# Optimization experiments

Hardware: AMD Instinct MI355X
Metric: run time of the kernel (lower is better)

Reference implementation:

```python
import jax, jax.numpy as jnp
import numpy as np

N_NODES = 50000
N_EDGES = 800000
N_GRAPHS = 128
HEADS = 4
NEG_SLOPE = 0.2


def gat_layer(x, src, dst, W, a_src, a_dst, b, n_nodes):
    # x: [N, Fin]; W: [Fin, H*Fout]; a_src/a_dst: [H, Fout]; b: [H*Fout]
    H, Fo = a_src.shape
    h = (x @ W).reshape(n_nodes, H, Fo)                      # [N, H, Fo]
    s_src = jnp.einsum('nhf,hf->nh', h, a_src)               # [N, H]
    s_dst = jnp.einsum('nhf,hf->nh', h, a_dst)               # [N, H]
    e = jax.nn.leaky_relu(s_src[src] + s_dst[dst], NEG_SLOPE)  # [E, H]
    # segment softmax over destination nodes
    emax = jax.ops.segment_max(e, dst, num_segments=n_nodes)
    ex = jnp.exp(e - emax[dst])
    denom = jax.ops.segment_sum(ex, dst, num_segments=n_nodes)
    alpha = ex / (denom[dst] + 1e-16)                        # [E, H]
    msg = h[src] * alpha[:, :, None]                         # [E, H, Fo]
    out = jax.ops.segment_sum(msg, dst, num_segments=n_nodes)
    return out.reshape(n_nodes, H * Fo) + b


def setup_inputs() -> dict:
    key = jax.random.key(0)
    ks = jax.random.split(key, 16)
    x = jax.random.normal(ks[0], (N_NODES, 128), dtype=jnp.float32)
    edge_index = jax.random.randint(ks[1], (2, N_EDGES), 0, N_NODES, dtype=jnp.int64 if jax.config.jax_enable_x64 else jnp.int32)
    batch_index = jnp.sort(jax.random.randint(ks[2], (N_NODES,), 0, N_GRAPHS))
    s = 0.1
    # layer 0: in=128 -> H=4, Fo=32  => hidden 128
    W0 = jax.random.normal(ks[3], (128, HEADS * 32), jnp.float32) * s
    a_src0 = jax.random.normal(ks[4], (HEADS, 32), jnp.float32) * s
    a_dst0 = jax.random.normal(ks[5], (HEADS, 32), jnp.float32) * s
    b0 = jnp.zeros((HEADS * 32,), jnp.float32)
    # layer 1: in=128 -> H=4, Fo=64 => hidden 256
    W1 = jax.random.normal(ks[6], (128, HEADS * 64), jnp.float32) * s
    a_src1 = jax.random.normal(ks[7], (HEADS, 64), jnp.float32) * s
    a_dst1 = jax.random.normal(ks[8], (HEADS, 64), jnp.float32) * s
    b1 = jnp.zeros((HEADS * 64,), jnp.float32)
    # layer 2: in=256 -> H=4, Fo=64 => hidden 256
    W2 = jax.random.normal(ks[9], (256, HEADS * 64), jnp.float32) * s
    a_src2 = jax.random.normal(ks[10], (HEADS, 64), jnp.float32) * s
    a_dst2 = jax.random.normal(ks[11], (HEADS, 64), jnp.float32) * s
    b2 = jnp.zeros((HEADS * 64,), jnp.float32)
    # readout linear: 512 -> 10
    Wout = jax.random.normal(ks[12], (512, 10), jnp.float32) * s
    bout = jnp.zeros((10,), jnp.float32)
    return dict(x=x, edge_index=edge_index, batch_index=batch_index,
                W0=W0, a_src0=a_src0, a_dst0=a_dst0, b0=b0,
                W1=W1, a_src1=a_src1, a_dst1=a_dst1, b1=b1,
                W2=W2, a_src2=a_src2, a_dst2=a_dst2, b2=b2,
                Wout=Wout, bout=bout)


def reference(x, edge_index, batch_index,
              W0, a_src0, a_dst0, b0,
              W1, a_src1, a_dst1, b1,
              W2, a_src2, a_dst2, b2,
              Wout, bout):
    n = x.shape[0]
    loops = jnp.arange(n, dtype=edge_index.dtype)
    src = jnp.concatenate([edge_index[0], loops])  # PyG add_self_loops
    dst = jnp.concatenate([edge_index[1], loops])
    h = jax.nn.relu(gat_layer(x, src, dst, W0, a_src0, a_dst0, b0, n))
    h = jax.nn.relu(gat_layer(h, src, dst, W1, a_src1, a_dst1, b1, n))
    h = jax.nn.relu(gat_layer(h, src, dst, W2, a_src2, a_dst2, b2, n))
    # global mean / max pool per graph
    ssum = jax.ops.segment_sum(h, batch_index, num_segments=N_GRAPHS)
    cnt = jax.ops.segment_sum(jnp.ones((n, 1), h.dtype), batch_index, num_segments=N_GRAPHS)
    gmean = ssum / jnp.maximum(cnt, 1.0)
    gmax = jax.ops.segment_max(h, batch_index, num_segments=N_GRAPHS)
    pooled = jnp.concatenate([gmean, gmax], axis=1)  # [G, 512]
    return pooled @ Wout + bout
```

## Files before the change

kernel.cpp:

```cpp
#include <hip/hip_runtime.h>
#include <cfloat>

#define N_NODES 50000
#define N_EDGES 800000
#define E_TOT   850000
#define NG      128
#define NH      4
#define CHUNK   782

typedef float f4 __attribute__((ext_vector_type(4)));
typedef float v4f __attribute__((ext_vector_type(4)));
typedef _Float16 h8v __attribute__((ext_vector_type(8)));

__global__ void count_dst_k(const int* __restrict__ ei, int* __restrict__ cnt) {
    int e = blockIdx.x * blockDim.x + threadIdx.x;
    if (e >= E_TOT) return;
    int d = (e < N_EDGES) ? ei[N_EDGES + e] : (e - N_EDGES);
    atomicAdd(&cnt[d], 1);
}

__global__ void scan_sums_k(const int* __restrict__ cnt, int* __restrict__ bsum) {
    int b = blockIdx.x;
    int start = b * CHUNK, end2 = min(start + CHUNK, N_NODES);
    int lane = threadIdx.x & 63, wv = threadIdx.x >> 6;
    int s = 0;
    for (int i = start + threadIdx.x; i < end2; i += 256) s += cnt[i];
    #pragma unroll
    for (int off = 32; off; off >>= 1) s += __shfl_xor(s, off);
    __shared__ int ws[4];
    if (lane == 0) ws[wv] = s;
    __syncthreads();
    if (threadIdx.x == 0) bsum[b] = ws[0] + ws[1] + ws[2] + ws[3];
}

__global__ void scan_off_k(int* __restrict__ bsum, int* __restrict__ row_ptr) {
    int lane = threadIdx.x;
    int v = bsum[lane];
    int s = v;
    #pragma unroll
    for (int off = 1; off < 64; off <<= 1) {
        int t = __shfl_up(s, off);
        if (lane >= off) s += t;
    }
    bsum[lane] = s - v;
    if (lane == 63) row_ptr[N_NODES] = s;
}

__global__ void scan_write_k(const int* __restrict__ cnt, const int* __restrict__ bsum,
                             int* __restrict__ row_ptr, int* __restrict__ cursor) {
    int b = blockIdx.x;
    int start = b * CHUNK, end2 = min(start + CHUNK, N_NODES);
    __shared__ int wsum[4];
    __shared__ int carry_sh;
    int lane = threadIdx.x & 63, wv = threadIdx.x >> 6;
    if (threadIdx.x == 0) carry_sh = bsum[b];
    __syncthreads();
    for (int base = start; base < end2; base += 256) {
        int i = base + threadIdx.x;
        int v = (i < end2) ? cnt[i] : 0;
        int s = v;
        #pragma unroll
        for (int off = 1; off < 64; off <<= 1) {
            int t = __shfl_up(s, off);
            if (lane >= off) s += t;
        }
        if (lane == 63) wsum[wv] = s;
        __syncthreads();
        int woff = 0;
        #pragma unroll
        for (int k = 0; k < 4; ++k) if (k < wv) woff += wsum[k];
        int carry = carry_sh;
        if (i < end2) { int rp = carry + woff + s - v; row_ptr[i] = rp; cursor[i] = rp; }
        __syncthreads();
        if (threadIdx.x == 0) carry_sh = carry + wsum[0] + wsum[1] + wsum[2] + wsum[3];
        __syncthreads();
    }
}

__global__ void fill_k(const int* __restrict__ ei, int* __restrict__ cursor,
                       int* __restrict__ col) {
    int e = blockIdx.x * blockDim.x + threadIdx.x;
    if (e >= E_TOT) return;
    int s, d;
    if (e < N_EDGES) { s = ei[e]; d = ei[N_EDGES + e]; }
    else { s = e - N_EDGES; d = s; }
    int slot = atomicAdd(&cursor[d], 1);
    col[slot] = s;
}

template<int K, int NOUT>
__global__ void pack_w_k(const float* __restrict__ W, _Float16* __restrict__ Wp) {
    constexpr int total = (NOUT / 16) * (K / 32) * 64;
    int t = blockIdx.x * blockDim.x + threadIdx.x;
    if (t >= total) return;
    int lane = t & 63;
    int rest = t >> 6;
    int ks = rest % (K / 32);
    int n  = rest / (K / 32);
    int colW = n * 16 + (lane & 15);
    int krow = ks * 32 + (lane >> 4) * 8;
    h8v v;
    #pragma unroll
    for (int j = 0; j < 8; ++j) v[j] = (_Float16)W[(size_t)(krow + j) * NOUT + colW];
    *(h8v*)(Wp + (size_t)t * 8) = v;
}

template<int K, int NOUT>
__global__ void pack_a_k(const float* __restrict__ W, const float* __restrict__ asrc,
                         const float* __restrict__ adst, _Float16* __restrict__ Wp) {
    constexpr int KS = K / 32;
    constexpr int NT = NOUT / 16;
    constexpr int Fo = NOUT / NH;
    int t = blockIdx.x * blockDim.x + threadIdx.x;
    if (t >= KS * 64) return;
    int ks = t >> 6, lane = t & 63;
    int colL = lane & 15;
    int krow = ks * 32 + ((lane >> 4) & 3) * 8;
    h8v v = {};
    if (colL < 8) {
        int hd = colL & 3;
        const float* av = (colL < 4) ? asrc : adst;
        #pragma unroll
        for (int j = 0; j < 8; ++j) {
            float s = 0.f;
            const float* wr = W + (size_t)(krow + j) * NOUT + hd * Fo;
            for (int f = 0; f < Fo; ++f) s += wr[f] * av[hd * Fo + f];
            v[j] = (_Float16)s;
        }
    }
    *(h8v*)(Wp + (size_t)((NT * KS + ks) * 64 + lane) * 8) = v;
}

template<int K, int NOUT, typename XT>
__global__ __launch_bounds__(256) void gemm_k(const XT* __restrict__ x,
                                              const _Float16* __restrict__ Wp,
                                              _Float16* __restrict__ outh,
                                              float* __restrict__ ssrc,
                                              float* __restrict__ sdst) {
    constexpr int SLICE = NOUT / 8;
    constexpr int KS  = K / 32;
    constexpr int NT  = NOUT / 16;
    constexpr int LK  = K + 8;
    __shared__ __align__(16) _Float16 xs[64 * LK];
    int row0 = blockIdx.x * 64;
    for (int seg = threadIdx.x; seg < 64 * K / 8; seg += 256) {
        int r = seg / (K / 8);
        int c = (seg % (K / 8)) * 8;
        h8v v = {};
        if (row0 + r < N_NODES) {
            if constexpr (sizeof(XT) == 2) {
                v = *(const h8v*)((const _Float16*)x + (size_t)(row0 + r) * K + c);
            } else {
                const float* xp = (const float*)x + (size_t)(row0 + r) * K + c;
                float4 a = *(const float4*)xp;
                float4 b = *(const float4*)(xp + 4);
                v[0] = (_Float16)a.x; v[1] = (_Float16)a.y;
                v[2] = (_Float16)a.z; v[3] = (_Float16)a.w;
                v[4] = (_Float16)b.x; v[5] = (_Float16)b.y;
                v[6] = (_Float16)b.z; v[7] = (_Float16)b.w;
            }
        }
        *(h8v*)(xs + r * LK + c) = v;
    }
    __syncthreads();
    int wv = threadIdx.x >> 6, lane = threadIdx.x & 63;
    int quad = lane >> 4, colL = lane & 15;
    int r0 = row0 + wv * 16;
    h8v afr[KS];
    #pragma unroll
    for (int ks = 0; ks < KS; ++ks)
        afr[ks] = *(const h8v*)(xs + (wv * 16 + colL) * LK + ks * 32 + quad * 8);
    const h8v* bp = (const h8v*)Wp;
    #pragma unroll
    for (int t = 0; t <= NT; ++t) {
        v4f acc = {};
        #pragma unroll
        for (int ks = 0; ks < KS; ++ks) {
            h8v bfr = bp[(size_t)(t * KS + ks) * 64 + lane];
            acc = __builtin_amdgcn_mfma_f32_16x16x32_f16(afr[ks], bfr, acc, 0, 0, 0);
        }
        if (t < NT) {
            int n0 = t * 16;
            int col = n0 + colL;
            int sl = n0 / SLICE;
            int so = col % SLICE;
            _Float16* op = outh + (size_t)sl * N_NODES * SLICE + so;
            #pragma unroll
            for (int reg = 0; reg < 4; ++reg) {
                int row = r0 + quad * 4 + reg;
                if (row < N_NODES) op[(size_t)row * SLICE] = (_Float16)acc[reg];
            }
        } else if (colL < 8) {
            int hd = colL & 3;
            float* sp = (colL < 4) ? ssrc : sdst;
            #pragma unroll
            for (int reg = 0; reg < 4; ++reg) {
                int row = r0 + quad * 4 + reg;
                if (row < N_NODES) sp[row * NH + hd] = acc[reg];
            }
        }
    }
}

__global__ __launch_bounds__(256) void alpha_k(const float* __restrict__ ssrc,
                                               const float* __restrict__ sdst,
                                               const int* __restrict__ row_ptr,
                                               const int* __restrict__ col,
                                               float* __restrict__ alpha) {
    int wv = threadIdx.x >> 6, lane = threadIdx.x & 63;
    int v = blockIdx.x * 4 + wv;
    if (v >= N_NODES) return;
    int hd = lane >> 4, lg = lane & 15;
    int beg = row_ptr[v], cnt = row_ptr[v + 1] - beg;
    float sdv = sdst[v * NH + hd];
    float* pl = alpha + (size_t)hd * E_TOT + beg;

    if (cnt <= 128) {
        float er[8];
        float m = -FLT_MAX;
        #pragma unroll
        for (int i = 0; i < 8; ++i) {
            int j = lg + i * 16;
            if (j < cnt) {
                int u = col[beg + j];
                float e = ssrc[u * NH + hd] + sdv;
                e = (e > 0.f) ? e : 0.2f * e;
                er[i] = e;
                m = fmaxf(m, e);
            }
        }
        #pragma unroll
        for (int off = 1; off < 16; off <<= 1) m = fmaxf(m, __shfl_xor(m, off));
        float den = 0.f;
        #pragma unroll
        for (int i = 0; i < 8; ++i) {
            int j = lg + i * 16;
            if (j < cnt) { float w = __expf(er[i] - m); er[i] = w; den += w; }
        }
        #pragma unroll
        for (int off = 1; off < 16; off <<= 1) den += __shfl_xor(den, off);
        float inv = 1.f / (den + 1e-16f);
        #pragma unroll
        for (int i = 0; i < 8; ++i) {
            int j = lg + i * 16;
            if (j < cnt) pl[j] = er[i] * inv;
        }
    } else {
        float m = -FLT_MAX;
        for (int j = lg; j < cnt; j += 16) {
            int u = col[beg + j];
            float e = ssrc[u * NH + hd] + sdv;
            e = (e > 0.f) ? e : 0.2f * e;
            m = fmaxf(m, e);
        }
        #pragma unroll
        for (int off = 1; off < 16; off <<= 1) m = fmaxf(m, __shfl_xor(m, off));
        float den = 0.f;
        for (int j = lg; j < cnt; j += 16) {
            int u = col[beg + j];
            float e = ssrc[u * NH + hd] + sdv;
            e = (e > 0.f) ? e : 0.2f * e;
            den += __expf(e - m);
        }
        #pragma unroll
        for (int off = 1; off < 16; off <<= 1) den += __shfl_xor(den, off);
        float inv = 1.f / (den + 1e-16f);
        for (int j = lg; j < cnt; j += 16) {
            int u = col[beg + j];
            float e = ssrc[u * NH + hd] + sdv;
            e = (e > 0.f) ? e : 0.2f * e;
            pl[j] = __expf(e - m) * inv;
        }
    }
}

template<int HFo, int SLICE, int LPN>
__global__ __launch_bounds__(256) void agg3_k(const _Float16* __restrict__ hh,
                                              const float* __restrict__ alpha,
                                              const int* __restrict__ row_ptr,
                                              const int* __restrict__ col,
                                              const float* __restrict__ bias,
                                              _Float16* __restrict__ outH) {
    constexpr int Fo   = HFo / NH;
    constexpr int NPW  = 64 / LPN;
    constexpr int NPB  = 4 * NPW;
    constexpr int CAPW = NPW * 32;
    __shared__ int   colS[4][CAPW];
    __shared__ float awS[4][CAPW];
    int s = blockIdx.x & 7;
    int g = blockIdx.x >> 3;
    int wv = threadIdx.x >> 6, lane = threadIdx.x & 63;
    int sub = lane / LPN, lq = lane % LPN;
    int vFirst = g * NPB + wv * NPW;
    if (vFirst >= N_NODES) return;
    int vCount = min(NPW, N_NODES - vFirst);
    int hd = (s * SLICE) / Fo;
    const float* ap = alpha + (size_t)hd * E_TOT;
    int begW = row_ptr[vFirst];
    int endW = row_ptr[vFirst + vCount];
    int len = endW - begW;
    bool active = sub < vCount;
    int v = vFirst + sub;
    int beg = 0, cnt = 0;
    if (active) { beg = row_ptr[v]; cnt = row_ptr[v + 1] - beg; }
    const _Float16* hp = hh + (size_t)s * N_NODES * SLICE + lq * 8;
    float acc[8] = {};

    if (len <= CAPW) {
        for (int t = lane; t < len; t += 64) {
            colS[wv][t] = col[begW + t];
            awS[wv][t]  = ap[begW + t];
        }
        __builtin_amdgcn_wave_barrier();
        int off = beg - begW;
        int j = 0;
        for (; j + 8 <= cnt; j += 8) {
            int u[8]; float w[8]; h8v hv[8];
            #pragma unroll
            for (int i = 0; i < 8; ++i) { u[i] = colS[wv][off + j + i]; w[i] = awS[wv][off + j + i]; }
            #pragma unroll
            for (int i = 0; i < 8; ++i) hv[i] = *(const h8v*)(hp + (size_t)u[i] * SLICE);
            #pragma unroll
            for (int i = 0; i < 8; ++i)
                #pragma unroll
                for (int c = 0; c < 8; ++c) acc[c] += w[i] * (float)hv[i][c];
        }
        for (; j < cnt; ++j) {
            int u = colS[wv][off + j];
            float w = awS[wv][off + j];
            h8v hv = *(const h8v*)(hp + (size_t)u * SLICE);
            #pragma unroll
            for (int c = 0; c < 8; ++c) acc[c] += w * (float)hv[c];
        }
    } else {
        const int*   cp = col + beg;
        const float* app = ap + beg;
        for (int j = 0; j < cnt; ++j) {
            int u = cp[j];
            float w = app[j];
            h8v hv = *(const h8v*)(hp + (size_t)u * SLICE);
            #pragma unroll
            for (int c = 0; c < 8; ++c) acc[c] += w * (float)hv[c];
        }
    }
    if (active) {
        int f0 = s * SLICE + lq * 8;
        h8v res;
        #pragma unroll
        for (int c = 0; c < 8; ++c) res[c] = (_Float16)fmaxf(acc[c] + bias[f0 + c], 0.f);
        *(h8v*)(outH + (size_t)v * HFo + f0) = res;
    }
}

__global__ void pool_k(const _Float16* __restrict__ h, const int* __restrict__ batch,
                       float* __restrict__ gsum, float* __restrict__ gmax) {
    int f = threadIdx.x;
    int n0 = blockIdx.x * 32;
    int nend = min(n0 + 32, N_NODES);
    int cur = -1;
    float sa = 0.f, ma = 0.f;
    for (int n = n0; n < nend; ++n) {
        int g = batch[n];
        float val = (float)h[(size_t)n * 256 + f];
        if (g != cur) {
            if (cur >= 0) {
                atomicAdd(&gsum[cur * 256 + f], sa);
                atomicMax((int*)&gmax[cur * 256 + f], __float_as_int(ma));
            }
            cur = g; sa = 0.f; ma = 0.f;
        }
        sa += val;
        ma = fmaxf(ma, val);
    }
    if (cur >= 0) {
        atomicAdd(&gsum[cur * 256 + f], sa);
        atomicMax((int*)&gmax[cur * 256 + f], __float_as_int(ma));
    }
}

__global__ void gcnt_k(const int* __restrict__ batch, int* __restrict__ gcnt) {
    int g = threadIdx.x;
    if (g >= NG) return;
    int lo = 0, hi = N_NODES;
    while (lo < hi) { int mid = (lo + hi) >> 1; if (batch[mid] < g) lo = mid + 1; else hi = mid; }
    int b0 = lo;
    lo = 0; hi = N_NODES;
    while (lo < hi) { int mid = (lo + hi) >> 1; if (batch[mid] < g + 1) lo = mid + 1; else hi = mid; }
    gcnt[g] = lo - b0;
}

__global__ void readout_k(const float* __restrict__ gsum, const float* __restrict__ gmax,
                          const int* __restrict__ gcnt, const float* __restrict__ Wout,
                          const float* __restrict__ bout, float* __restrict__ out) {
    int g = blockIdx.x, lane = threadIdx.x;
    float inv = 1.f / fmaxf((float)gcnt[g], 1.f);
    float acc[10];
    #pragma unroll
    for (int j = 0; j < 10; ++j) acc[j] = 0.f;
    for (int f = lane; f < 512; f += 64) {
        float p = (f < 256) ? gsum[g * 256 + f] * inv : gmax[g * 256 + (f - 256)];
        #pragma unroll
        for (int j = 0; j < 10; ++j) acc[j] += p * Wout[f * 10 + j];
    }
    #pragma unroll
    for (int j = 0; j < 10; ++j) {
        float a = acc[j];
        #pragma unroll
        for (int off = 32; off; off >>= 1) a += __shfl_xor(a, off);
        if (lane == 0) out[g * 10 + j] = a + bout[j];
    }
}

extern "C" void kernel_launch(void* const* d_in, const int* in_sizes, int n_in,
                              void* d_out, int out_size, void* d_ws, size_t ws_size,
                              hipStream_t stream) {
    const float* x    = (const float*)d_in[0];
    const int*   ei   = (const int*)d_in[1];
    const int*   batch= (const int*)d_in[2];
    const float* W0   = (const float*)d_in[3];
    const float* as0  = (const float*)d_in[4];
    const float* ad0  = (const float*)d_in[5];
    const float* b0   = (const float*)d_in[6];
    const float* W1   = (const float*)d_in[7];
    const float* as1  = (const float*)d_in[8];
    const float* ad1  = (const float*)d_in[9];
    const float* b1   = (const float*)d_in[10];
    const float* W2   = (const float*)d_in[11];
    const float* as2  = (const float*)d_in[12];
    const float* ad2  = (const float*)d_in[13];
    const float* b2   = (const float*)d_in[14];
    const float* Wout = (const float*)d_in[15];
    const float* bout = (const float*)d_in[16];
    float* out = (float*)d_out;

    char* ws = (char*)d_ws;
    size_t o = 0;
    auto take = [&](size_t bytes) { size_t r = o; o += (bytes + 255) & ~(size_t)255; return r; };
    size_t cnt_o  = take((size_t)N_NODES * 4);
    size_t gsum_o = take((size_t)NG * 256 * 4);
    size_t gmax_o = take((size_t)NG * 256 * 4);
    size_t gcnt_o = take((size_t)NG * 4);
    size_t zero_bytes = o;
    size_t rp_o   = take((size_t)(N_NODES + 1) * 4);
    size_t cur_o  = take((size_t)N_NODES * 4);
    size_t bsum_o = take((size_t)64 * 4);
    size_t col_o  = take((size_t)E_TOT * 4);
    size_t ssrc_o = take((size_t)N_NODES * NH * 4);
    size_t sdst_o = take((size_t)N_NODES * NH * 4);
    size_t alp_o  = take((size_t)NH * E_TOT * 4);
    size_t hh_o   = take((size_t)N_NODES * 256 * 2);
    size_t bufH_o = take((size_t)N_NODES * 256 * 2);
    size_t wp0_o  = take((size_t)(8 + 1) * 4 * 64 * 8 * 2);
    size_t wp1_o  = take((size_t)(16 + 1) * 4 * 64 * 8 * 2);
    size_t wp2_o  = take((size_t)(16 + 1) * 8 * 64 * 8 * 2);

    int*      cnt    = (int*)(ws + cnt_o);
    float*    gsum   = (float*)(ws + gsum_o);
    float*    gmax   = (float*)(ws + gmax_o);
    int*      gcnt   = (int*)(ws + gcnt_o);
    int*      row_ptr= (int*)(ws + rp_o);
    int*      cursor = (int*)(ws + cur_o);
    int*      bsum   = (int*)(ws + bsum_o);
    int*      col    = (int*)(ws + col_o);
    float*    ssrc   = (float*)(ws + ssrc_o);
    float*    sdst   = (float*)(ws + sdst_o);
    float*    alpha  = (float*)(ws + alp_o);
    _Float16* hH     = (_Float16*)(ws + hh_o);
    _Float16* bufH   = (_Float16*)(ws + bufH_o);
    _Float16* Wp0    = (_Float16*)(ws + wp0_o);
    _Float16* Wp1    = (_Float16*)(ws + wp1_o);
    _Float16* Wp2    = (_Float16*)(ws + wp2_o);

    (void)hipMemsetAsync(ws, 0, zero_bytes, stream);

    count_dst_k<<<(E_TOT + 255) / 256, 256, 0, stream>>>(ei, cnt);
    scan_sums_k<<<64, 256, 0, stream>>>(cnt, bsum);
    scan_off_k<<<1, 64, 0, stream>>>(bsum, row_ptr);
    scan_write_k<<<64, 256, 0, stream>>>(cnt, bsum, row_ptr, cursor);
    fill_k<<<(E_TOT + 255) / 256, 256, 0, stream>>>(ei, cursor, col);

    pack_w_k<128, 128><<<8, 256, 0, stream>>>(W0, Wp0);
    pack_w_k<128, 256><<<16, 256, 0, stream>>>(W1, Wp1);
    pack_w_k<256, 256><<<32, 256, 0, stream>>>(W2, Wp2);
    pack_a_k<128, 128><<<1, 256, 0, stream>>>(W0, as0, ad0, Wp0);
    pack_a_k<128, 256><<<1, 256, 0, stream>>>(W1, as1, ad1, Wp1);
    pack_a_k<256, 256><<<2, 256, 0, stream>>>(W2, as2, ad2, Wp2);

    int gemm_grid  = (N_NODES + 63) / 64;
    int alpha_grid = (N_NODES + 3) / 4;
    int agg128_grid = 8 * ((N_NODES + 127) / 128);
    int agg256_grid = 8 * ((N_NODES + 63) / 64);

    gemm_k<128, 128, float><<<gemm_grid, 256, 0, stream>>>(x, Wp0, hH, ssrc, sdst);
    alpha_k<<<alpha_grid, 256, 0, stream>>>(ssrc, sdst, row_ptr, col, alpha);
    agg3_k<128, 16, 2><<<agg128_grid, 256, 0, stream>>>(hH, alpha, row_ptr, col, b0, bufH);

    gemm_k<128, 256, _Float16><<<gemm_grid, 256, 0, stream>>>(bufH, Wp1, hH, ssrc, sdst);
    alpha_k<<<alpha_grid, 256, 0, stream>>>(ssrc, sdst, row_ptr, col, alpha);
    agg3_k<256, 32, 4><<<agg256_grid, 256, 0, stream>>>(hH, alpha, row_ptr, col, b1, bufH);

    gemm_k<256, 256, _Float16><<<gemm_grid, 256, 0, stream>>>(bufH, Wp2, hH, ssrc, sdst);
    alpha_k<<<alpha_grid, 256, 0, stream>>>(ssrc, sdst, row_ptr, col, alpha);
    agg3_k<256, 32, 4><<<agg256_grid, 256, 0, stream>>>(hH, alpha, row_ptr, col, b2, bufH);

    pool_k<<<(N_NODES + 31) / 32, 256, 0, stream>>>(bufH, batch, gsum, gmax);
    gcnt_k<<<1, 128, 0, stream>>>(batch, gcnt);
    readout_k<<<NG, 64, 0, stream>>>(gsum, gmax, gcnt, Wout, bout, out);
}
```

Before: 525.8 us.

## Build CSR via two-pass bucketed fill with shared-memory per-node cursors

Replaces the per-node global atomic cursor fill with two passes. The first pass scatters packed (local dst, src) pairs into 64-node buckets using one global atomic per bucket. The second pass does a per-bucket local sort with shared-memory atomics to write col. The aim is to cut the cost of scattered global atomics and writes. In exchange it adds a temp buffer, two extra launches and more contention on the 782 bucket counters.

New measurement: 697.7 us. 1.33x slower.

```diff
diff --git a/kernel.cpp b/kernel.cpp
--- a/kernel.cpp
+++ b/kernel.cpp
@@ -7,6 +7,7 @@
 #define NG      128
 #define NH      4
 #define CHUNK   782
+#define NB      782
 
 typedef float f4 __attribute__((ext_vector_type(4)));
 typedef float v4f __attribute__((ext_vector_type(4)));
@@ -47,7 +48,7 @@
 }
 
 __global__ void scan_write_k(const int* __restrict__ cnt, const int* __restrict__ bsum,
-                             int* __restrict__ row_ptr, int* __restrict__ cursor) {
+                             int* __restrict__ row_ptr) {
     int b = blockIdx.x;
     int start = b * CHUNK, end2 = min(start + CHUNK, N_NODES);
     __shared__ int wsum[4];
@@ -70,22 +71,46 @@
         #pragma unroll
         for (int k = 0; k < 4; ++k) if (k < wv) woff += wsum[k];
         int carry = carry_sh;
-        if (i < end2) { int rp = carry + woff + s - v; row_ptr[i] = rp; cursor[i] = rp; }
+        if (i < end2) row_ptr[i] = carry + woff + s - v;
         __syncthreads();
         if (threadIdx.x == 0) carry_sh = carry + wsum[0] + wsum[1] + wsum[2] + wsum[3];
         __syncthreads();
     }
 }
 
-__global__ void fill_k(const int* __restrict__ ei, int* __restrict__ cursor,
-                       int* __restrict__ col) {
+__global__ void binit_k(const int* __restrict__ row_ptr, int* __restrict__ bcur) {
+    int b = blockIdx.x * blockDim.x + threadIdx.x;
+    if (b < NB) bcur[b] = row_ptr[b << 6];
+}
+
+__global__ void fill_a_k(const int* __restrict__ ei, int* __restrict__ bcur,
+                         int* __restrict__ tmp) {
     int e = blockIdx.x * blockDim.x + threadIdx.x;
     if (e >= E_TOT) return;
     int s, d;
     if (e < N_EDGES) { s = ei[e]; d = ei[N_EDGES + e]; }
     else { s = e - N_EDGES; d = s; }
-    int slot = atomicAdd(&cursor[d], 1);
-    col[slot] = s;
+    int b = d >> 6;
+    int slot = atomicAdd(&bcur[b], 1);
+    tmp[slot] = ((d & 63) << 16) | s;
+}
+
+__global__ void fill_b_k(const int* __restrict__ row_ptr, const int* __restrict__ tmp,
+                         int* __restrict__ col) {
+    __shared__ int lcur[64];
+    int b = blockIdx.x;
+    int n0 = b << 6;
+    int n1 = min(n0 + 64, N_NODES);
+    int base = row_ptr[n0], end2 = row_ptr[n1];
+    if (threadIdx.x < n1 - n0) lcur[threadIdx.x] = row_ptr[n0 + threadIdx.x];
+    __syncthreads();
+    for (int i = base + threadIdx.x; i < end2; i += 256) {
+        int v = tmp[i];
+        int rel = v >> 16;
+        int s = v & 0xFFFF;
+        int slot = atomicAdd(&lcur[rel], 1);
+        col[slot] = s;
+    }
 }
 
 template<int K, int NOUT>
@@ -442,8 +467,9 @@
     size_t gcnt_o = take((size_t)NG * 4);
     size_t zero_bytes = o;
     size_t rp_o   = take((size_t)(N_NODES + 1) * 4);
-    size_t cur_o  = take((size_t)N_NODES * 4);
     size_t bsum_o = take((size_t)64 * 4);
+    size_t bcur_o = take((size_t)NB * 4);
+    size_t tmp_o  = take((size_t)E_TOT * 4);
     size_t col_o  = take((size_t)E_TOT * 4);
     size_t ssrc_o = take((size_t)N_NODES * NH * 4);
     size_t sdst_o = take((size_t)N_NODES * NH * 4);
@@ -459,8 +485,9 @@
     float*    gmax   = (float*)(ws + gmax_o);
     int*      gcnt   = (int*)(ws + gcnt_o);
     int*      row_ptr= (int*)(ws + rp_o);
-    int*      cursor = (int*)(ws + cur_o);
     int*      bsum   = (int*)(ws + bsum_o);
+    int*      bcur   = (int*)(ws + bcur_o);
+    int*      tmp    = (int*)(ws + tmp_o);
     int*      col    = (int*)(ws + col_o);
     float*    ssrc   = (float*)(ws + ssrc_o);
     float*    sdst   = (float*)(ws + sdst_o);
@@ -476,8 +503,10 @@
     count_dst_k<<<(E_TOT + 255) / 256, 256, 0, stream>>>(ei, cnt);
     scan_sums_k<<<64, 256, 0, stream>>>(cnt, bsum);
     scan_off_k<<<1, 64, 0, stream>>>(bsum, row_ptr);
-    scan_write_k<<<64, 256, 0, stream>>>(cnt, bsum, row_ptr, cursor);
-    fill_k<<<(E_TOT + 255) / 256, 256, 0, stream>>>(ei, cursor, col);
+    scan_write_k<<<64, 256, 0, stream>>>(cnt, bsum, row_ptr);
+    binit_k<<<(NB + 255) / 256, 256, 0, stream>>>(row_ptr, bcur);
+    fill_a_k<<<(E_TOT + 255) / 256, 256, 0, stream>>>(ei, bcur, tmp);
+    fill_b_k<<<NB, 256, 0, stream>>>(row_ptr, tmp, col);
 
     pack_w_k<128, 128><<<8, 256, 0, stream>>>(W0, Wp0);
     pack_w_k<128, 256><<<16, 256, 0, stream>>>(W1, Wp1);
```
